# Kernel tuning notes

Measured on AMD Instinct MI355X. Metric: run time of the kernel, lower is better.

The kernel has to match this reference:

```python
import jax, jax.numpy as jnp
import numpy as np

N_NODES = 40000
N_EDGES = 640000
IN_CH = 11
HID = 128
OUT_CH = 1
NUM_LEVELS = 2


def _lin(x, w, b):
    # torch nn.Linear: w is [out, in]
    return x @ w.T + b


def _conv(x, src, dst, w1, b1, w2, b2, w3, b3):
    # Reconstructed MLMPNNConv forward: embed, then NUM_LEVELS rounds of
    # scatter-add message passing (message = x_j), concat levels, project.
    h = jax.nn.relu(_lin(x, w1, b1))  # [N, HID]
    outs = []
    for _ in range(NUM_LEVELS):
        agg = jax.ops.segment_sum(h[src], dst, num_segments=N_NODES)  # gather + scatter-add
        h = jax.nn.relu(_lin(agg, w2, b2))
        outs.append(h)
    return _lin(jnp.concatenate(outs, axis=-1), w3, b3)  # [N, out]


def setup_inputs() -> dict:
    key = jax.random.key(0)
    ks = jax.random.split(key, 16)
    d = {}
    d["x"] = jax.random.normal(ks[0], (N_NODES, IN_CH), dtype=jnp.float32)
    d["edge_index"] = jax.random.randint(ks[1], (2, N_EDGES), 0, N_NODES, dtype=jnp.int32)
    s = 0.05
    # conv 0: lin1 IN->HID, lin2 HID->HID, lin3 2*HID->HID
    d["c0_w1"] = jax.random.normal(ks[2], (HID, IN_CH)) * s
    d["c0_b1"] = jnp.zeros((HID,), jnp.float32)
    d["c0_w2"] = jax.random.normal(ks[3], (HID, HID)) * s
    d["c0_b2"] = jnp.zeros((HID,), jnp.float32)
    d["c0_w3"] = jax.random.normal(ks[4], (HID, HID * NUM_LEVELS)) * s
    d["c0_b3"] = jnp.zeros((HID,), jnp.float32)
    # conv 1: lin1 HID->HID
    d["c1_w1"] = jax.random.normal(ks[5], (HID, HID)) * s
    d["c1_b1"] = jnp.zeros((HID,), jnp.float32)
    d["c1_w2"] = jax.random.normal(ks[6], (HID, HID)) * s
    d["c1_b2"] = jnp.zeros((HID,), jnp.float32)
    d["c1_w3"] = jax.random.normal(ks[7], (HID, HID * NUM_LEVELS)) * s
    d["c1_b3"] = jnp.zeros((HID,), jnp.float32)
    # head
    d["f_w1"] = jax.random.normal(ks[8], (HID, HID)) * s
    d["f_b1"] = jnp.zeros((HID,), jnp.float32)
    d["f_w2"] = jax.random.normal(ks[9], (OUT_CH, HID)) * s
    d["f_b2"] = jnp.zeros((OUT_CH,), jnp.float32)
    return d


def reference(x, edge_index,
              c0_w1, c0_b1, c0_w2, c0_b2, c0_w3, c0_b3,
              c1_w1, c1_b1, c1_w2, c1_b2, c1_w3, c1_b3,
              f_w1, f_b1, f_w2, f_b2):
    src, dst = edge_index[0], edge_index[1]
    h = _conv(x, src, dst, c0_w1, c0_b1, c0_w2, c0_b2, c0_w3, c0_b3)
    h = _conv(h, src, dst, c1_w1, c1_b1, c1_w2, c1_b2, c1_w3, c1_b3)
    h = jax.nn.relu(_lin(h, f_w1, f_b1))
    return _lin(h, f_w2, f_b2)  # [N, 1]
```

## Files before the change

### kernel.cpp

```cpp
#include <hip/hip_runtime.h>
#include <hip/hip_fp16.h>

#define NN 40000
#define NE 640000
#define HID 128
#define EB ((NE + 255) / 256)
#define ECAP 1536

typedef __attribute__((ext_vector_type(8)))  short short8;
typedef __attribute__((ext_vector_type(4)))  short short4v;
typedef __attribute__((ext_vector_type(16))) float floatx16;
typedef unsigned int uint;

__device__ __forceinline__ short f2bf(float f) {
    union { float f; unsigned u; } c; c.f = f;
    unsigned u = c.u;
    unsigned r = (u + 0x7FFF + ((u >> 16) & 1)) >> 16;
    return (short)r;
}
__device__ __forceinline__ float bf2f(short h) {
    union { unsigned u; float f; } c;
    c.u = ((unsigned)(unsigned short)h) << 16;
    return c.f;
}
__device__ __forceinline__ float2 h2f2(uint u) {
    union { uint u; __half2 h; } c; c.u = u;
    return __half22float2(c.h);
}
__device__ __forceinline__ void splits(float f, short* hi, short* lo) {
    short h = f2bf(f);
    *hi = h;
    *lo = f2bf(f - bf2f(h));
}
__device__ __forceinline__ void unpack8(uint4 a, uint4 b, short8* h, short8* l) {
    short8 H, L;
    H[0] = (short)(a.x >> 16); L[0] = (short)a.x;
    H[1] = (short)(a.y >> 16); L[1] = (short)a.y;
    H[2] = (short)(a.z >> 16); L[2] = (short)a.z;
    H[3] = (short)(a.w >> 16); L[3] = (short)a.w;
    H[4] = (short)(b.x >> 16); L[4] = (short)b.x;
    H[5] = (short)(b.y >> 16); L[5] = (short)b.y;
    H[6] = (short)(b.z >> 16); L[6] = (short)b.z;
    H[7] = (short)(b.w >> 16); L[7] = (short)b.w;
    *h = H; *l = L;
}

__device__ __forceinline__ int wswz(int o, int k) {
    int chunk = k >> 4, half = (k >> 3) & 1, j = k & 7;
    int ct = o >> 5, m31 = o & 31;
    int lane = half * 32 + m31;
    return (((chunk * 4 + ct) * 64 + lane) * 8 + j);
}

#define ACC4(u, A, B)                                                     \
    { float2 f0 = h2f2(u.x), f1 = h2f2(u.y);                              \
      float2 f2 = h2f2(u.z), f3 = h2f2(u.w);                              \
      A.x += f0.x; A.y += f0.y; A.z += f1.x; A.w += f1.y;                 \
      B.x += f2.x; B.y += f2.y; B.z += f3.x; B.w += f3.y; }

#define GBODY(IDX)                                                        \
        for (; e + 8 <= hi; e += 8) {                                     \
            int s0 = IDX(e + sub);     int s1 = IDX(e + 2 + sub);         \
            int s2 = IDX(e + 4 + sub); int s3 = IDX(e + 6 + sub);         \
            uint4 u0 = hp[(size_t)s0 * 16 + c16];                         \
            uint4 u1 = hp[(size_t)s1 * 16 + c16];                         \
            uint4 u2 = hp[(size_t)s2 * 16 + c16];                         \
            uint4 u3 = hp[(size_t)s3 * 16 + c16];                         \
            ACC4(u0, a0, a1); ACC4(u1, b0, b1);                           \
            ACC4(u2, c0, c1); ACC4(u3, d0, d1);                           \
        }                                                                 \
        for (; e + 2 <= hi; e += 2) {                                     \
            int s0 = IDX(e + sub);                                        \
            uint4 u0 = hp[(size_t)s0 * 16 + c16];                         \
            ACC4(u0, a0, a1);                                             \
        }                                                                 \
        if (sub == 0 && e < hi) {                                         \
            int s0 = IDX(e);                                              \
            uint4 u0 = hp[(size_t)s0 * 16 + c16];                         \
            ACC4(u0, b0, b1);                                             \
        }

#define IDXS(j) sE[(j)]
#define IDXG(j) esrc[lo0 + (j)]

__global__ __launch_bounds__(256, 4) void fused_gather_lin_kernel(
    const __half* __restrict__ h, const int* __restrict__ row_ptr,
    const int* __restrict__ esrc, const uint* __restrict__ Wq,
    const float* __restrict__ bias, __half* __restrict__ out)
{
    __shared__ short sAh[4096];
    __shared__ short sAl[4096];
    __shared__ int   sE[ECAP];
    __shared__ int   sRP[33];
    __shared__ int   sCtr;
    const int t   = threadIdx.x;
    const int r0  = blockIdx.x * 32;
    const int c16 = t & 15;
    const int sub = (t >> 4) & 1;
    const uint4* hp = (const uint4*)h;

    if (t == 0) sCtr = 0;
    if (t < 33) sRP[t] = row_ptr[r0 + t];
    __syncthreads();
    const int lo0 = sRP[0];
    const int nE  = sRP[32] - lo0;
    const int nStage = nE < ECAP ? nE : ECAP;
    for (int i = t; i < nStage; i += 256) sE[i] = esrc[lo0 + i];
    __syncthreads();
    const bool fast = (nE <= ECAP);

    for (;;) {
        int n = 0;
        if ((t & 31) == 0) n = atomicAdd(&sCtr, 1);
        n = __shfl(n, 0, 32);
        if (n >= 32) break;
        const int lo = sRP[n] - lo0, hi = sRP[n + 1] - lo0;
        float4 a0 = make_float4(0,0,0,0), a1 = make_float4(0,0,0,0);
        float4 b0 = make_float4(0,0,0,0), b1 = make_float4(0,0,0,0);
        float4 c0 = make_float4(0,0,0,0), c1 = make_float4(0,0,0,0);
        float4 d0 = make_float4(0,0,0,0), d1 = make_float4(0,0,0,0);
        int e = lo;
        if (fast) { GBODY(IDXS) } else { GBODY(IDXG) }
        float4 v0, v1;
        v0.x = (a0.x + b0.x) + (c0.x + d0.x);
        v0.y = (a0.y + b0.y) + (c0.y + d0.y);
        v0.z = (a0.z + b0.z) + (c0.z + d0.z);
        v0.w = (a0.w + b0.w) + (c0.w + d0.w);
        v1.x = (a1.x + b1.x) + (c1.x + d1.x);
        v1.y = (a1.y + b1.y) + (c1.y + d1.y);
        v1.z = (a1.z + b1.z) + (c1.z + d1.z);
        v1.w = (a1.w + b1.w) + (c1.w + d1.w);
        v0.x += __shfl_down(v0.x, 16, 32);
        v0.y += __shfl_down(v0.y, 16, 32);
        v0.z += __shfl_down(v0.z, 16, 32);
        v0.w += __shfl_down(v0.w, 16, 32);
        v1.x += __shfl_down(v1.x, 16, 32);
        v1.y += __shfl_down(v1.y, 16, 32);
        v1.z += __shfl_down(v1.z, 16, 32);
        v1.w += __shfl_down(v1.w, 16, 32);
        if (sub == 0) {
            short8 H, L;
            short hh, ll;
            splits(v0.x, &hh, &ll); H[0] = hh; L[0] = ll;
            splits(v0.y, &hh, &ll); H[1] = hh; L[1] = ll;
            splits(v0.z, &hh, &ll); H[2] = hh; L[2] = ll;
            splits(v0.w, &hh, &ll); H[3] = hh; L[3] = ll;
            splits(v1.x, &hh, &ll); H[4] = hh; L[4] = ll;
            splits(v1.y, &hh, &ll); H[5] = hh; L[5] = ll;
            splits(v1.z, &hh, &ll); H[6] = hh; L[6] = ll;
            splits(v1.w, &hh, &ll); H[7] = hh; L[7] = ll;
            const int off = c16 * 256 + n * 8;
            *(short8*)(sAh + off) = H;
            *(short8*)(sAl + off) = L;
        }
    }
    __syncthreads();

    const int wv   = t >> 6;
    const int lane = t & 63;
    const int m31  = lane & 31;
    const int half = lane >> 5;
    floatx16 acc;
    #pragma unroll
    for (int i = 0; i < 16; ++i) acc[i] = 0.f;
    #pragma unroll
    for (int c = 0; c < 8; ++c) {
        short8 ah = *(const short8*)(sAh + (c * 2 + half) * 256 + m31 * 8);
        short8 al = *(const short8*)(sAl + (c * 2 + half) * 256 + m31 * 8);
        const uint* wr = Wq + ((size_t)(c * 4 + wv) * 64 + lane) * 8;
        uint4 w0 = *(const uint4*)(wr);
        uint4 w1 = *(const uint4*)(wr + 4);
        short8 bh, bl;
        unpack8(w0, w1, &bh, &bl);
        acc = __builtin_amdgcn_mfma_f32_32x32x16_bf16(ah, bh, acc, 0, 0, 0);
        acc = __builtin_amdgcn_mfma_f32_32x32x16_bf16(al, bh, acc, 0, 0, 0);
        acc = __builtin_amdgcn_mfma_f32_32x32x16_bf16(ah, bl, acc, 0, 0, 0);
    }
    const int col = wv * 32 + m31;
    const float bb = bias[col];
    #pragma unroll
    for (int reg = 0; reg < 16; ++reg) {
        int row = (reg & 3) + 8 * (reg >> 2) + 4 * half;
        float v = fmaxf(acc[reg] + bb, 0.f);
        out[(size_t)(r0 + row) * HID + col] = __float2half(v);
    }
}

template<int PHASES, bool RELU>
__global__ __launch_bounds__(256, 4) void lin32_kernel(
    const __half* __restrict__ X0, const __half* __restrict__ X1,
    const uint* __restrict__ Wq, const float* __restrict__ bias,
    __half* __restrict__ out)
{
    __shared__ short sAh[PHASES * 4096];
    __shared__ short sAl[PHASES * 4096];
    const int t  = threadIdx.x;
    const int r0 = blockIdx.x * 32;

    #pragma unroll
    for (int i = 0; i < PHASES * 4; ++i) {
        int v = t + 256 * i;
        const __half* Xp = (PHASES == 2 && v >= 1024) ? X1 : X0;
        int vv  = v & 1023;
        int row = vv >> 5, q = vv & 31;
        uint2 u = *(const uint2*)(Xp + (size_t)(r0 + row) * 128 + q * 4);
        float2 f0 = h2f2(u.x), f1 = h2f2(u.y);
        int kk  = ((PHASES == 2) ? (v >> 10) * 128 : 0) + q * 4;
        int off = (kk >> 3) * 256 + row * 8 + (q & 1) * 4;
        short4v hi, lo;
        short hh, ll;
        splits(f0.x, &hh, &ll); hi.x = hh; lo.x = ll;
        splits(f0.y, &hh, &ll); hi.y = hh; lo.y = ll;
        splits(f1.x, &hh, &ll); hi.z = hh; lo.z = ll;
        splits(f1.y, &hh, &ll); hi.w = hh; lo.w = ll;
        *(short4v*)(sAh + off) = hi;
        *(short4v*)(sAl + off) = lo;
    }
    __syncthreads();

    const int wv   = t >> 6;
    const int lane = t & 63;
    const int m31  = lane & 31;
    const int half = lane >> 5;
    floatx16 acc;
    #pragma unroll
    for (int i = 0; i < 16; ++i) acc[i] = 0.f;
    #pragma unroll
    for (int c = 0; c < PHASES * 8; ++c) {
        short8 ah = *(const short8*)(sAh + (c * 2 + half) * 256 + m31 * 8);
        short8 al = *(const short8*)(sAl + (c * 2 + half) * 256 + m31 * 8);
        const uint* wr = Wq + ((size_t)(c * 4 + wv) * 64 + lane) * 8;
        uint4 w0 = *(const uint4*)(wr);
        uint4 w1 = *(const uint4*)(wr + 4);
        short8 bh, bl;
        unpack8(w0, w1, &bh, &bl);
        acc = __builtin_amdgcn_mfma_f32_32x32x16_bf16(ah, bh, acc, 0, 0, 0);
        acc = __builtin_amdgcn_mfma_f32_32x32x16_bf16(al, bh, acc, 0, 0, 0);
        acc = __builtin_amdgcn_mfma_f32_32x32x16_bf16(ah, bl, acc, 0, 0, 0);
    }
    const int col = wv * 32 + m31;
    const float bb = bias[col];
    #pragma unroll
    for (int reg = 0; reg < 16; ++reg) {
        int row = (reg & 3) + 8 * (reg >> 2) + 4 * half;
        float v = acc[reg] + bb;
        if (RELU) v = fmaxf(v, 0.f);
        out[(size_t)(r0 + row) * HID + col] = __float2half(v);
    }
}

__global__ __launch_bounds__(256, 3) void cat_head_kernel(
    const __half* __restrict__ X0, const __half* __restrict__ X1,
    const uint* __restrict__ Wq, const float* __restrict__ bias,
    const float* __restrict__ f2, const float* __restrict__ f2b,
    float* __restrict__ out)
{
    __shared__ short sAh[8192];
    __shared__ short sAl[8192];
    __shared__ float gbuf[32 * 129];
    const int t  = threadIdx.x;
    const int r0 = blockIdx.x * 32;

    #pragma unroll
    for (int i = 0; i < 8; ++i) {
        int v = t + 256 * i;
        const __half* Xp = (v >= 1024) ? X1 : X0;
        int vv  = v & 1023;
        int row = vv >> 5, q = vv & 31;
        uint2 u = *(const uint2*)(Xp + (size_t)(r0 + row) * 128 + q * 4);
        float2 f0 = h2f2(u.x), f1 = h2f2(u.y);
        int kk  = (v >> 10) * 128 + q * 4;
        int off = (kk >> 3) * 256 + row * 8 + (q & 1) * 4;
        short4v hi, lo;
        short hh, ll;
        splits(f0.x, &hh, &ll); hi.x = hh; lo.x = ll;
        splits(f0.y, &hh, &ll); hi.y = hh; lo.y = ll;
        splits(f1.x, &hh, &ll); hi.z = hh; lo.z = ll;
        splits(f1.y, &hh, &ll); hi.w = hh; lo.w = ll;
        *(short4v*)(sAh + off) = hi;
        *(short4v*)(sAl + off) = lo;
    }
    __syncthreads();

    const int wv   = t >> 6;
    const int lane = t & 63;
    const int m31  = lane & 31;
    const int half = lane >> 5;
    floatx16 acc;
    #pragma unroll
    for (int i = 0; i < 16; ++i) acc[i] = 0.f;
    #pragma unroll
    for (int c = 0; c < 16; ++c) {
        short8 ah = *(const short8*)(sAh + (c * 2 + half) * 256 + m31 * 8);
        short8 al = *(const short8*)(sAl + (c * 2 + half) * 256 + m31 * 8);
        const uint* wr = Wq + ((size_t)(c * 4 + wv) * 64 + lane) * 8;
        uint4 w0 = *(const uint4*)(wr);
        uint4 w1 = *(const uint4*)(wr + 4);
        short8 bh, bl;
        unpack8(w0, w1, &bh, &bl);
        acc = __builtin_amdgcn_mfma_f32_32x32x16_bf16(ah, bh, acc, 0, 0, 0);
        acc = __builtin_amdgcn_mfma_f32_32x32x16_bf16(al, bh, acc, 0, 0, 0);
        acc = __builtin_amdgcn_mfma_f32_32x32x16_bf16(ah, bl, acc, 0, 0, 0);
    }
    const int col = wv * 32 + m31;
    const float bb = bias[col];
    #pragma unroll
    for (int reg = 0; reg < 16; ++reg) {
        int row = (reg & 3) + 8 * (reg >> 2) + 4 * half;
        gbuf[row * 129 + col] = fmaxf(acc[reg] + bb, 0.f);
    }
    __syncthreads();

    const int node = t >> 3;
    const int seg  = t & 7;
    const float* gr = gbuf + node * 129 + seg * 16;
    float a = 0.f;
    #pragma unroll
    for (int i = 0; i < 16; ++i) a += gr[i] * f2[seg * 16 + i];
    a += __shfl_down(a, 4, 8);
    a += __shfl_down(a, 2, 8);
    a += __shfl_down(a, 1, 8);
    if (seg == 0) out[r0 + node] = a + f2b[0];
}

__global__ __launch_bounds__(256) void prep_kernel(
    const float* __restrict__ c0w2, const float* __restrict__ c1w2,
    const float* __restrict__ c1w1, const float* __restrict__ c0w3,
    const float* __restrict__ c0b3, const float* __restrict__ c1b1,
    const float* __restrict__ fw1,  const float* __restrict__ c1w3,
    const float* __restrict__ c1b3, const float* __restrict__ fb1,
    const int* __restrict__ dst, int* __restrict__ cnt, int* __restrict__ rank,
    uint* __restrict__ wp, uint* __restrict__ p_Wa, uint* __restrict__ p_Wb,
    float* __restrict__ f_ba, float* __restrict__ f_bb)
{
    const int b = blockIdx.x;
    const int t = threadIdx.x;
    if (b < 128) {
        int i = b * 256 + t;
        const float* src = (i < 16384) ? c0w2 : c1w2;
        int off = (i < 16384) ? 0 : 16384;
        int L = i - off;
        int o = L >> 7, k = L & 127;
        short hh, ll;
        splits(src[L], &hh, &ll);
        wp[off + wswz(o, k)] = ((uint)(unsigned short)hh << 16) | (uint)(unsigned short)ll;
    } else if (b < 384) {
        const bool isA = (b < 256);
        const int o = b - (isA ? 128 : 256);
        const float* A   = isA ? c1w1 : fw1;
        const float* B   = isA ? c0w3 : c1w3;
        const float* bi  = isA ? c0b3 : c1b3;
        const float* bo  = isA ? c1b1 : fb1;
        uint*  W  = isA ? p_Wa : p_Wb;
        float* bb = isA ? f_ba : f_bb;
        const float* Ar = A + o * 128;
        float s = 0.f;
        for (int j = 0; j < 128; ++j) s += Ar[j] * B[j * 256 + t];
        short hh, ll;
        splits(s, &hh, &ll);
        W[wswz(o, t)] = ((uint)(unsigned short)hh << 16) | (uint)(unsigned short)ll;
        if (t == 0) {
            float sb = 0.f;
            for (int j = 0; j < 128; ++j) sb += Ar[j] * bi[j];
            bb[o] = sb + bo[o];
        }
    } else {
        int e = (b - 384) * 256 + t;
        if (e < NE) rank[e] = atomicAdd(&cnt[dst[e]], 1);
    }
}

#define SCHUNK 40
__global__ __launch_bounds__(1024) void scan_kernel(
    const int* __restrict__ cnt, int* __restrict__ row_ptr)
{
    __shared__ int s[1024];
    const int t = threadIdx.x;
    const int base = t * SCHUNK;
    int sum = 0;
    if (base < NN) {
        int n = min(SCHUNK, NN - base);
        #pragma unroll 8
        for (int j = 0; j < n; ++j) sum += cnt[base + j];
    }
    s[t] = sum;
    __syncthreads();
    #pragma unroll
    for (int off = 1; off < 1024; off <<= 1) {
        int x = (t >= off) ? s[t - off] : 0;
        __syncthreads();
        s[t] += x;
        __syncthreads();
    }
    int run = (t == 0) ? 0 : s[t - 1];
    if (base < NN) {
        int n = min(SCHUNK, NN - base);
        for (int j = 0; j < n; ++j) {
            int v = cnt[base + j];
            row_ptr[base + j] = run;
            run += v;
        }
    }
    if (t == 1023) row_ptr[NN] = s[1023];
}

__global__ __launch_bounds__(256) void fill_embed_kernel(
    const int* __restrict__ src, const int* __restrict__ dst,
    const int* __restrict__ row_ptr, const int* __restrict__ rank,
    int* __restrict__ esrc,
    const float* __restrict__ x, const float* __restrict__ w1,
    const float* __restrict__ b1, __half* __restrict__ h0)
{
    const int b = blockIdx.x;
    const int t = threadIdx.x;
    if (b < EB) {
        int e = b * 256 + t;
        if (e < NE) {
            int d = dst[e];
            esrc[row_ptr[d] + rank[e]] = src[e];
        }
    } else {
        __shared__ float xs[2][88];
        const int hf = t >> 7;
        const int m  = t & 127;
        const int r0 = (b - EB) * 16 + hf * 8;
        for (int i = m; i < 88; i += 128) {
            int r = i / 11, k = i - r * 11;
            xs[hf][i] = x[(size_t)(r0 + r) * 11 + k];
        }
        __syncthreads();
        float acc[8] = {};
        const float* Wm = w1 + m * 11;
        #pragma unroll
        for (int k = 0; k < 11; ++k) {
            float w = Wm[k];
            #pragma unroll
            for (int r = 0; r < 8; ++r) acc[r] += xs[hf][r * 11 + k] * w;
        }
        const float bias = b1[m];
        #pragma unroll
        for (int r = 0; r < 8; ++r) {
            float v = fmaxf(acc[r] + bias, 0.f);
            h0[(size_t)(r0 + r) * HID + m] = __float2half(v);
        }
    }
}

extern "C" void kernel_launch(void* const* d_in, const int* in_sizes, int n_in,
                              void* d_out, int out_size, void* d_ws, size_t ws_size,
                              hipStream_t stream)
{
    const float* x     = (const float*)d_in[0];
    const int*   eidx  = (const int*)d_in[1];
    const float* c0_w1 = (const float*)d_in[2],  *c0_b1 = (const float*)d_in[3];
    const float* c0_w2 = (const float*)d_in[4],  *c0_b2 = (const float*)d_in[5];
    const float* c0_w3 = (const float*)d_in[6],  *c0_b3 = (const float*)d_in[7];
    const float* c1_w1 = (const float*)d_in[8],  *c1_b1 = (const float*)d_in[9];
    const float* c1_w2 = (const float*)d_in[10], *c1_b2 = (const float*)d_in[11];
    const float* c1_w3 = (const float*)d_in[12], *c1_b3 = (const float*)d_in[13];
    const float* f_w1  = (const float*)d_in[14], *f_b1  = (const float*)d_in[15];
    const float* f_w2  = (const float*)d_in[16], *f_b2  = (const float*)d_in[17];
    const int* src = eidx;
    const int* dst = eidx + NE;
    float* out = (float*)d_out;

    const size_t BUF = (size_t)NN * HID;
    __half* bA = (__half*)d_ws;
    __half* bB = bA + BUF;
    __half* bC = bB + BUF;
    int* row_ptr  = (int*)(bC + BUF);
    int* cnt      = row_ptr + (NN + 1);
    int* esrc     = cnt + NN;
    uint* wp      = (uint*)(esrc + NE);

    uint* p_c0w2 = wp + 0;
    uint* p_c1w2 = wp + 16384;
    uint* p_Wa   = wp + 32768;
    uint* p_Wb   = wp + 65536;
    float* f_ba  = (float*)(wp + 98304);
    float* f_bb  = f_ba + 128;

    int* rank = (int*)bC;

    const int nbl = (NN + 31) / 32;

    (void)hipMemsetAsync(cnt, 0, NN * sizeof(int), stream);
    prep_kernel<<<384 + EB, 256, 0, stream>>>(
        c0_w2, c1_w2, c1_w1, c0_w3, c0_b3, c1_b1,
        f_w1, c1_w3, c1_b3, f_b1, dst, cnt, rank, wp, p_Wa, p_Wb, f_ba, f_bb);
    scan_kernel<<<1, 1024, 0, stream>>>(cnt, row_ptr);
    fill_embed_kernel<<<EB + 2500, 256, 0, stream>>>(
        src, dst, row_ptr, rank, esrc, x, c0_w1, c0_b1, bA);

    fused_gather_lin_kernel<<<nbl, 256, 0, stream>>>(bA, row_ptr, esrc, p_c0w2, c0_b2, bB);
    fused_gather_lin_kernel<<<nbl, 256, 0, stream>>>(bB, row_ptr, esrc, p_c0w2, c0_b2, bC);
    lin32_kernel<2, true><<<nbl, 256, 0, stream>>>(bB, bC, p_Wa, f_ba, bA);

    fused_gather_lin_kernel<<<nbl, 256, 0, stream>>>(bA, row_ptr, esrc, p_c1w2, c1_b2, bB);
    fused_gather_lin_kernel<<<nbl, 256, 0, stream>>>(bB, row_ptr, esrc, p_c1w2, c1_b2, bC);
    cat_head_kernel<<<nbl, 256, 0, stream>>>(bB, bC, p_Wb, f_bb, f_w2, f_b2, out);
}
```

Baseline: 298.7 us.

## Fuse second-level gather+linear with concat projection/head kernel

Merges the second message-passing level with the following concat projection (and with the head for conv1) into one kernel. The level-2 result stays in shared memory as split bf16 instead of being written to global memory and reread, and level-1 rows are loaded directly. This removes two launches and an intermediate buffer round trip. In exchange, shared memory per block grows, so the head variant runs at lower occupancy.

Measured after the change: 302.4 us. No clear change (+1.3%).

```diff
diff --git a/kernel.cpp b/kernel.cpp
--- a/kernel.cpp
+++ b/kernel.cpp
@@ -83,6 +83,78 @@
 #define IDXS(j) sE[(j)]
 #define IDXG(j) esrc[lo0 + (j)]
 
+#define GATHER_PHASE                                                          \
+    if (t == 0) sCtr = 0;                                                     \
+    if (t < 33) sRP[t] = row_ptr[r0 + t];                                     \
+    __syncthreads();                                                          \
+    const int lo0 = sRP[0];                                                   \
+    const int nE  = sRP[32] - lo0;                                            \
+    const int nStage = nE < ECAP ? nE : ECAP;                                 \
+    for (int i = t; i < nStage; i += 256) sE[i] = esrc[lo0 + i];              \
+    __syncthreads();                                                          \
+    const bool fast = (nE <= ECAP);                                           \
+    for (;;) {                                                                \
+        int n = 0;                                                            \
+        if ((t & 31) == 0) n = atomicAdd(&sCtr, 1);                           \
+        n = __shfl(n, 0, 32);                                                 \
+        if (n >= 32) break;                                                   \
+        const int lo = sRP[n] - lo0, hi = sRP[n + 1] - lo0;                   \
+        float4 a0 = make_float4(0,0,0,0), a1 = make_float4(0,0,0,0);          \
+        float4 b0 = make_float4(0,0,0,0), b1 = make_float4(0,0,0,0);          \
+        float4 c0 = make_float4(0,0,0,0), c1 = make_float4(0,0,0,0);          \
+        float4 d0 = make_float4(0,0,0,0), d1 = make_float4(0,0,0,0);          \
+        int e = lo;                                                           \
+        if (fast) { GBODY(IDXS) } else { GBODY(IDXG) }                        \
+        float4 v0, v1;                                                        \
+        v0.x = (a0.x + b0.x) + (c0.x + d0.x);                                 \
+        v0.y = (a0.y + b0.y) + (c0.y + d0.y);                                 \
+        v0.z = (a0.z + b0.z) + (c0.z + d0.z);                                 \
+        v0.w = (a0.w + b0.w) + (c0.w + d0.w);                                 \
+        v1.x = (a1.x + b1.x) + (c1.x + d1.x);                                 \
+        v1.y = (a1.y + b1.y) + (c1.y + d1.y);                                 \
+        v1.z = (a1.z + b1.z) + (c1.z + d1.z);                                 \
+        v1.w = (a1.w + b1.w) + (c1.w + d1.w);                                 \
+        v0.x += __shfl_down(v0.x, 16, 32);                                    \
+        v0.y += __shfl_down(v0.y, 16, 32);                                    \
+        v0.z += __shfl_down(v0.z, 16, 32);                                    \
+        v0.w += __shfl_down(v0.w, 16, 32);                                    \
+        v1.x += __shfl_down(v1.x, 16, 32);                                    \
+        v1.y += __shfl_down(v1.y, 16, 32);                                    \
+        v1.z += __shfl_down(v1.z, 16, 32);                                    \
+        v1.w += __shfl_down(v1.w, 16, 32);                                    \
+        if (sub == 0) {                                                       \
+            short8 H, L;                                                      \
+            short hh, ll;                                                     \
+            splits(v0.x, &hh, &ll); H[0] = hh; L[0] = ll;                     \
+            splits(v0.y, &hh, &ll); H[1] = hh; L[1] = ll;                     \
+            splits(v0.z, &hh, &ll); H[2] = hh; L[2] = ll;                     \
+            splits(v0.w, &hh, &ll); H[3] = hh; L[3] = ll;                     \
+            splits(v1.x, &hh, &ll); H[4] = hh; L[4] = ll;                     \
+            splits(v1.y, &hh, &ll); H[5] = hh; L[5] = ll;                     \
+            splits(v1.z, &hh, &ll); H[6] = hh; L[6] = ll;                     \
+            splits(v1.w, &hh, &ll); H[7] = hh; L[7] = ll;                     \
+            const int off = c16 * 256 + n * 8;                                \
+            *(short8*)(sAh + off) = H;                                        \
+            *(short8*)(sAl + off) = L;                                        \
+        }                                                                     \
+    }                                                                         \
+    __syncthreads();
+
+#define MFMA_LOOP(NC, WQ, ACC)                                                \
+    _Pragma("unroll")                                                         \
+    for (int c = 0; c < NC; ++c) {                                            \
+        short8 ah = *(const short8*)(sAh + (c * 2 + half) * 256 + m31 * 8);   \
+        short8 al = *(const short8*)(sAl + (c * 2 + half) * 256 + m31 * 8);   \
+        const uint* wr = WQ + ((size_t)(c * 4 + wv) * 64 + lane) * 8;         \
+        uint4 w0 = *(const uint4*)(wr);                                       \
+        uint4 w1 = *(const uint4*)(wr + 4);                                   \
+        short8 bh, bl;                                                        \
+        unpack8(w0, w1, &bh, &bl);                                            \
+        ACC = __builtin_amdgcn_mfma_f32_32x32x16_bf16(ah, bh, ACC, 0, 0, 0);  \
+        ACC = __builtin_amdgcn_mfma_f32_32x32x16_bf16(al, bh, ACC, 0, 0, 0);  \
+        ACC = __builtin_amdgcn_mfma_f32_32x32x16_bf16(ah, bl, ACC, 0, 0, 0);  \
+    }
+
 __global__ __launch_bounds__(256, 4) void fused_gather_lin_kernel(
     const __half* __restrict__ h, const int* __restrict__ row_ptr,
     const int* __restrict__ esrc, const uint* __restrict__ Wq,
@@ -99,62 +171,7 @@
     const int sub = (t >> 4) & 1;
     const uint4* hp = (const uint4*)h;
 
-    if (t == 0) sCtr = 0;
-    if (t < 33) sRP[t] = row_ptr[r0 + t];
-    __syncthreads();
-    const int lo0 = sRP[0];
-    const int nE  = sRP[32] - lo0;
-    const int nStage = nE < ECAP ? nE : ECAP;
-    for (int i = t; i < nStage; i += 256) sE[i] = esrc[lo0 + i];
-    __syncthreads();
-    const bool fast = (nE <= ECAP);
-
-    for (;;) {
-        int n = 0;
-        if ((t & 31) == 0) n = atomicAdd(&sCtr, 1);
-        n = __shfl(n, 0, 32);
-        if (n >= 32) break;
-        const int lo = sRP[n] - lo0, hi = sRP[n + 1] - lo0;
-        float4 a0 = make_float4(0,0,0,0), a1 = make_float4(0,0,0,0);
-        float4 b0 = make_float4(0,0,0,0), b1 = make_float4(0,0,0,0);
-        float4 c0 = make_float4(0,0,0,0), c1 = make_float4(0,0,0,0);
-        float4 d0 = make_float4(0,0,0,0), d1 = make_float4(0,0,0,0);
-        int e = lo;
-        if (fast) { GBODY(IDXS) } else { GBODY(IDXG) }
-        float4 v0, v1;
-        v0.x = (a0.x + b0.x) + (c0.x + d0.x);
-        v0.y = (a0.y + b0.y) + (c0.y + d0.y);
-        v0.z = (a0.z + b0.z) + (c0.z + d0.z);
-        v0.w = (a0.w + b0.w) + (c0.w + d0.w);
-        v1.x = (a1.x + b1.x) + (c1.x + d1.x);
-        v1.y = (a1.y + b1.y) + (c1.y + d1.y);
-        v1.z = (a1.z + b1.z) + (c1.z + d1.z);
-        v1.w = (a1.w + b1.w) + (c1.w + d1.w);
-        v0.x += __shfl_down(v0.x, 16, 32);
-        v0.y += __shfl_down(v0.y, 16, 32);
-        v0.z += __shfl_down(v0.z, 16, 32);
-        v0.w += __shfl_down(v0.w, 16, 32);
-        v1.x += __shfl_down(v1.x, 16, 32);
-        v1.y += __shfl_down(v1.y, 16, 32);
-        v1.z += __shfl_down(v1.z, 16, 32);
-        v1.w += __shfl_down(v1.w, 16, 32);
-        if (sub == 0) {
-            short8 H, L;
-            short hh, ll;
-            splits(v0.x, &hh, &ll); H[0] = hh; L[0] = ll;
-            splits(v0.y, &hh, &ll); H[1] = hh; L[1] = ll;
-            splits(v0.z, &hh, &ll); H[2] = hh; L[2] = ll;
-            splits(v0.w, &hh, &ll); H[3] = hh; L[3] = ll;
-            splits(v1.x, &hh, &ll); H[4] = hh; L[4] = ll;
-            splits(v1.y, &hh, &ll); H[5] = hh; L[5] = ll;
-            splits(v1.z, &hh, &ll); H[6] = hh; L[6] = ll;
-            splits(v1.w, &hh, &ll); H[7] = hh; L[7] = ll;
-            const int off = c16 * 256 + n * 8;
-            *(short8*)(sAh + off) = H;
-            *(short8*)(sAl + off) = L;
-        }
-    }
-    __syncthreads();
+    GATHER_PHASE
 
     const int wv   = t >> 6;
     const int lane = t & 63;
@@ -163,19 +180,7 @@
     floatx16 acc;
     #pragma unroll
     for (int i = 0; i < 16; ++i) acc[i] = 0.f;
-    #pragma unroll
-    for (int c = 0; c < 8; ++c) {
-        short8 ah = *(const short8*)(sAh + (c * 2 + half) * 256 + m31 * 8);
-        short8 al = *(const short8*)(sAl + (c * 2 + half) * 256 + m31 * 8);
-        const uint* wr = Wq + ((size_t)(c * 4 + wv) * 64 + lane) * 8;
-        uint4 w0 = *(const uint4*)(wr);
-        uint4 w1 = *(const uint4*)(wr + 4);
-        short8 bh, bl;
-        unpack8(w0, w1, &bh, &bl);
-        acc = __builtin_amdgcn_mfma_f32_32x32x16_bf16(ah, bh, acc, 0, 0, 0);
-        acc = __builtin_amdgcn_mfma_f32_32x32x16_bf16(al, bh, acc, 0, 0, 0);
-        acc = __builtin_amdgcn_mfma_f32_32x32x16_bf16(ah, bl, acc, 0, 0, 0);
-    }
+    MFMA_LOOP(8, Wq, acc)
     const int col = wv * 32 + m31;
     const float bb = bias[col];
     #pragma unroll
@@ -186,27 +191,62 @@
     }
 }
 
-template<int PHASES, bool RELU>
-__global__ __launch_bounds__(256, 4) void lin32_kernel(
-    const __half* __restrict__ X0, const __half* __restrict__ X1,
-    const uint* __restrict__ Wq, const float* __restrict__ bias,
-    __half* __restrict__ out)
-{
-    __shared__ short sAh[PHASES * 4096];
-    __shared__ short sAl[PHASES * 4096];
-    const int t  = threadIdx.x;
-    const int r0 = blockIdx.x * 32;
+template<bool HEAD>
+__global__ __launch_bounds__(256, HEAD ? 3 : 4) void gather2_fused_kernel(
+    const __half* __restrict__ h, const int* __restrict__ row_ptr,
+    const int* __restrict__ esrc, const uint* __restrict__ Wq,
+    const float* __restrict__ bias, const uint* __restrict__ Wq2,
+    const float* __restrict__ bias2, __half* __restrict__ outA,
+    const float* __restrict__ f2, const float* __restrict__ f2b,
+    float* __restrict__ outF)
+{
+    __shared__ short sAh[8192];
+    __shared__ short sAl[8192];
+    __shared__ __align__(16) char upool[HEAD ? (32 * 129 * 4) : (ECAP * 4)];
+    __shared__ int   sRP[33];
+    __shared__ int   sCtr;
+    int*   sE   = (int*)upool;
+    float* gbuf = (float*)upool;
+    const int t   = threadIdx.x;
+    const int r0  = blockIdx.x * 32;
+    const int c16 = t & 15;
+    const int sub = (t >> 4) & 1;
+    const uint4* hp = (const uint4*)h;
+
+    GATHER_PHASE
+
+    const int wv   = t >> 6;
+    const int lane = t & 63;
+    const int m31  = lane & 31;
+    const int half = lane >> 5;
+    const int col  = wv * 32 + m31;
+
+    {
+        floatx16 acc1;
+        #pragma unroll
+        for (int i = 0; i < 16; ++i) acc1[i] = 0.f;
+        MFMA_LOOP(8, Wq, acc1)
+        const float bb = bias[col];
+        #pragma unroll
+        for (int reg = 0; reg < 16; ++reg) {
+            int row = (reg & 3) + 8 * (reg >> 2) + 4 * half;
+            float v = fmaxf(acc1[reg] + bb, 0.f);
+            short hh, ll;
+            splits(v, &hh, &ll);
+            int off2 = (16 + (col >> 3)) * 256 + row * 8 + (col & 7);
+            sAh[off2] = hh;
+            sAl[off2] = ll;
+        }
+    }
+    __syncthreads();
 
     #pragma unroll
-    for (int i = 0; i < PHASES * 4; ++i) {
+    for (int i = 0; i < 4; ++i) {
         int v = t + 256 * i;
-        const __half* Xp = (PHASES == 2 && v >= 1024) ? X1 : X0;
-        int vv  = v & 1023;
-        int row = vv >> 5, q = vv & 31;
-        uint2 u = *(const uint2*)(Xp + (size_t)(r0 + row) * 128 + q * 4);
+        int row = v >> 5, q = v & 31;
+        uint2 u = *(const uint2*)((const __half*)h + (size_t)(r0 + row) * 128 + q * 4);
         float2 f0 = h2f2(u.x), f1 = h2f2(u.y);
-        int kk  = ((PHASES == 2) ? (v >> 10) * 128 : 0) + q * 4;
-        int off = (kk >> 3) * 256 + row * 8 + (q & 1) * 4;
+        int off = (q >> 1) * 256 + row * 8 + (q & 1) * 4;
         short4v hi, lo;
         short hh, ll;
         splits(f0.x, &hh, &ll); hi.x = hh; lo.x = ll;
@@ -218,109 +258,37 @@
     }
     __syncthreads();
 
-    const int wv   = t >> 6;
-    const int lane = t & 63;
-    const int m31  = lane & 31;
-    const int half = lane >> 5;
-    floatx16 acc;
+    floatx16 acc2;
     #pragma unroll
-    for (int i = 0; i < 16; ++i) acc[i] = 0.f;
-    #pragma unroll
-    for (int c = 0; c < PHASES * 8; ++c) {
-        short8 ah = *(const short8*)(sAh + (c * 2 + half) * 256 + m31 * 8);
-        short8 al = *(const short8*)(sAl + (c * 2 + half) * 256 + m31 * 8);
-        const uint* wr = Wq + ((size_t)(c * 4 + wv) * 64 + lane) * 8;
-        uint4 w0 = *(const uint4*)(wr);
-        uint4 w1 = *(const uint4*)(wr + 4);
-        short8 bh, bl;
-        unpack8(w0, w1, &bh, &bl);
-        acc = __builtin_amdgcn_mfma_f32_32x32x16_bf16(ah, bh, acc, 0, 0, 0);
-        acc = __builtin_amdgcn_mfma_f32_32x32x16_bf16(al, bh, acc, 0, 0, 0);
-        acc = __builtin_amdgcn_mfma_f32_32x32x16_bf16(ah, bl, acc, 0, 0, 0);
-    }
-    const int col = wv * 32 + m31;
-    const float bb = bias[col];
-    #pragma unroll
-    for (int reg = 0; reg < 16; ++reg) {
-        int row = (reg & 3) + 8 * (reg >> 2) + 4 * half;
-        float v = acc[reg] + bb;
-        if (RELU) v = fmaxf(v, 0.f);
-        out[(size_t)(r0 + row) * HID + col] = __float2half(v);
-    }
-}
-
-__global__ __launch_bounds__(256, 3) void cat_head_kernel(
-    const __half* __restrict__ X0, const __half* __restrict__ X1,
-    const uint* __restrict__ Wq, const float* __restrict__ bias,
-    const float* __restrict__ f2, const float* __restrict__ f2b,
-    float* __restrict__ out)
-{
-    __shared__ short sAh[8192];
-    __shared__ short sAl[8192];
-    __shared__ float gbuf[32 * 129];
-    const int t  = threadIdx.x;
-    const int r0 = blockIdx.x * 32;
-
-    #pragma unroll
-    for (int i = 0; i < 8; ++i) {
-        int v = t + 256 * i;
-        const __half* Xp = (v >= 1024) ? X1 : X0;
-        int vv  = v & 1023;
-        int row = vv >> 5, q = vv & 31;
-        uint2 u = *(const uint2*)(Xp + (size_t)(r0 + row) * 128 + q * 4);
-        float2 f0 = h2f2(u.x), f1 = h2f2(u.y);
-        int kk  = (v >> 10) * 128 + q * 4;
-        int off = (kk >> 3) * 256 + row * 8 + (q & 1) * 4;
-        short4v hi, lo;
-        short hh, ll;
-        splits(f0.x, &hh, &ll); hi.x = hh; lo.x = ll;
-        splits(f0.y, &hh, &ll); hi.y = hh; lo.y = ll;
-        splits(f1.x, &hh, &ll); hi.z = hh; lo.z = ll;
-        splits(f1.y, &hh, &ll); hi.w = hh; lo.w = ll;
-        *(short4v*)(sAh + off) = hi;
-        *(short4v*)(sAl + off) = lo;
-    }
-    __syncthreads();
-
-    const int wv   = t >> 6;
-    const int lane = t & 63;
-    const int m31  = lane & 31;
-    const int half = lane >> 5;
-    floatx16 acc;
-    #pragma unroll
-    for (int i = 0; i < 16; ++i) acc[i] = 0.f;
-    #pragma unroll
-    for (int c = 0; c < 16; ++c) {
-        short8 ah = *(const short8*)(sAh + (c * 2 + half) * 256 + m31 * 8);
-        short8 al = *(const short8*)(sAl + (c * 2 + half) * 256 + m31 * 8);
-        const uint* wr = Wq + ((size_t)(c * 4 + wv) * 64 + lane) * 8;
-        uint4 w0 = *(const uint4*)(wr);
-        uint4 w1 = *(const uint4*)(wr + 4);
-        short8 bh, bl;
-        unpack8(w0, w1, &bh, &bl);
-        acc = __builtin_amdgcn_mfma_f32_32x32x16_bf16(ah, bh, acc, 0, 0, 0);
-        acc = __builtin_amdgcn_mfma_f32_32x32x16_bf16(al, bh, acc, 0, 0, 0);
-        acc = __builtin_amdgcn_mfma_f32_32x32x16_bf16(ah, bl, acc, 0, 0, 0);
-    }
-    const int col = wv * 32 + m31;
-    const float bb = bias[col];
-    #pragma unroll
-    for (int reg = 0; reg < 16; ++reg) {
-        int row = (reg & 3) + 8 * (reg >> 2) + 4 * half;
-        gbuf[row * 129 + col] = fmaxf(acc[reg] + bb, 0.f);
-    }
-    __syncthreads();
-
-    const int node = t >> 3;
-    const int seg  = t & 7;
-    const float* gr = gbuf + node * 129 + seg * 16;
-    float a = 0.f;
-    #pragma unroll
-    for (int i = 0; i < 16; ++i) a += gr[i] * f2[seg * 16 + i];
-    a += __shfl_down(a, 4, 8);
-    a += __shfl_down(a, 2, 8);
-    a += __shfl_down(a, 1, 8);
-    if (seg == 0) out[r0 + node] = a + f2b[0];
+    for (int i = 0; i < 16; ++i) acc2[i] = 0.f;
+    MFMA_LOOP(16, Wq2, acc2)
+
+    const float b2 = bias2[col];
+    if (!HEAD) {
+        #pragma unroll
+        for (int reg = 0; reg < 16; ++reg) {
+            int row = (reg & 3) + 8 * (reg >> 2) + 4 * half;
+            float v = fmaxf(acc2[reg] + b2, 0.f);
+            outA[(size_t)(r0 + row) * HID + col] = __float2half(v);
+        }
+    } else {
+        #pragma unroll
+        for (int reg = 0; reg < 16; ++reg) {
+            int row = (reg & 3) + 8 * (reg >> 2) + 4 * half;
+            gbuf[row * 129 + col] = fmaxf(acc2[reg] + b2, 0.f);
+        }
+        __syncthreads();
+        const int node = t >> 3;
+        const int seg  = t & 7;
+        const float* gr = gbuf + node * 129 + seg * 16;
+        float a = 0.f;
+        #pragma unroll
+        for (int i = 0; i < 16; ++i) a += gr[i] * f2[seg * 16 + i];
+        a += __shfl_down(a, 4, 8);
+        a += __shfl_down(a, 2, 8);
+        a += __shfl_down(a, 1, 8);
+        if (seg == 0) outF[r0 + node] = a + f2b[0];
+    }
 }
 
 __global__ __launch_bounds__(256) void prep_kernel(
@@ -493,10 +461,10 @@
         src, dst, row_ptr, rank, esrc, x, c0_w1, c0_b1, bA);
 
     fused_gather_lin_kernel<<<nbl, 256, 0, stream>>>(bA, row_ptr, esrc, p_c0w2, c0_b2, bB);
-    fused_gather_lin_kernel<<<nbl, 256, 0, stream>>>(bB, row_ptr, esrc, p_c0w2, c0_b2, bC);
-    lin32_kernel<2, true><<<nbl, 256, 0, stream>>>(bB, bC, p_Wa, f_ba, bA);
+    gather2_fused_kernel<false><<<nbl, 256, 0, stream>>>(
+        bB, row_ptr, esrc, p_c0w2, c0_b2, p_Wa, f_ba, bA, nullptr, nullptr, nullptr);
 
     fused_gather_lin_kernel<<<nbl, 256, 0, stream>>>(bA, row_ptr, esrc, p_c1w2, c1_b2, bB);
-    fused_gather_lin_kernel<<<nbl, 256, 0, stream>>>(bB, row_ptr, esrc, p_c1w2, c1_b2, bC);
-    cat_head_kernel<<<nbl, 256, 0, stream>>>(bB, bC, p_Wb, f_bb, f_w2, f_b2, out);
-}
+    gather2_fused_kernel<true><<<nbl, 256, 0, stream>>>(
+        bB, row_ptr, esrc, p_c1w2, c1_b2, p_Wb, f_bb, nullptr, f_w2, f_b2, out);
+}
```
